# Performance work log

Hardware: AMD Instinct MI355X
Metric: run time of the kernel (lower is better)

The kernel has to match this reference:

```python
import jax, jax.numpy as jnp
import numpy as np

C = 8            # feat_channel
B, K, H, W = 8, 32, 128, 128
CW = (C + 2) * C + C + C * C + C + C + 1  # 169


def setup_inputs() -> dict:
    key = jax.random.key(0)
    k1, k2, k3, k4, k5 = jax.random.split(key, 5)
    seg_feat = jax.random.normal(k1, (B, C, H, W), jnp.float32)
    conv_weight = jax.random.normal(k2, (B, CW, H, W), jnp.float32) * 0.1
    mask = jax.random.randint(k3, (B, K), 0, 2).astype(jnp.int32)
    ind = jax.random.randint(k4, (B, K), 0, H * W).astype(jnp.int64)
    target = jax.random.uniform(k5, (B, K, H, W), jnp.float32)
    return {"seg_feat": seg_feat, "conv_weight": conv_weight, "mask": mask,
            "ind": ind, "target": target}


def reference(seg_feat, conv_weight, mask, ind, target):
    b, c, h, w = seg_feat.shape
    k = ind.shape[1]
    # gather_feature(conv_weight, ind, use_transform=True): [B,CW,H,W] -> [B,HW,CW] -> gather -> [B,K,CW]
    cw = conv_weight.reshape(b, -1, h * w).transpose(0, 2, 1)
    weight = jnp.take_along_axis(cw, ind[:, :, None], axis=1)  # [B,K,CW]

    sizes = [(c + 2) * c, c, c * c, c, c, 1]
    splits = np.cumsum(sizes)[:-1]
    c1w, c1b, c2w, c2b, c3w, c3b = jnp.split(weight, splits, axis=-1)
    c1w = c1w.reshape(b, k, c, c + 2)   # per-object 1x1 conv weights
    c2w = c2w.reshape(b, k, c, c)
    c3w = c3w.reshape(b, k, 1, c)

    x = (ind % w).astype(jnp.float32)
    y = (ind // w).astype(jnp.float32)
    y_grid, x_grid = jnp.meshgrid(jnp.arange(h, dtype=jnp.float32),
                                  jnp.arange(w, dtype=jnp.float32), indexing='ij')
    x_rel = (x_grid[None, None] - x[:, :, None, None]) / w   # [B,K,H,W]
    y_rel = (y_grid[None, None] - y[:, :, None, None]) / h

    feat = jnp.concatenate([
        jnp.broadcast_to(seg_feat[:, None], (b, k, c, h, w)),
        x_rel[:, :, None], y_rel[:, :, None]], axis=2)       # [B,K,C+2,H,W]

    feat = jax.nn.relu(jnp.einsum('bkoc,bkchw->bkohw', c1w, feat) + c1b[..., None, None])
    feat = jax.nn.relu(jnp.einsum('bkoc,bkchw->bkohw', c2w, feat) + c2b[..., None, None])
    pred = jax.nn.sigmoid(jnp.einsum('bkoc,bkchw->bkohw', c3w, feat)
                          + c3b[..., None, None])[:, :, 0]    # [B,K,H,W]

    m = mask.astype(jnp.float32)[:, :, None, None]
    p = pred * m
    t = target * m
    smooth = 1.0
    inter = jnp.sum(p * t, axis=(1, 2, 3))
    denom = jnp.sum(p * p, axis=(1, 2, 3)) + jnp.sum(t * t, axis=(1, 2, 3)) + smooth
    per_img = 1.0 - (2.0 * inter + smooth) / denom
    return jnp.mean(per_img)   # sum over images / valid_batch_size (all valid)
```

## Files before the change

### kernel.cpp

```cpp
#include <hip/hip_runtime.h>

#define C8     8
#define KOBJ   32
#define BIMG   8
#define WW     128
#define HH     128
#define HWPIX  16384
#define CWN    169
#define PIX    8
#define GRIDX  8
#define NBLK_PER_B (KOBJ * GRIDX)
#define NXCD   8


__global__ __launch_bounds__(256) void mask_head_kernel(
    const float* __restrict__ seg_feat,
    const float* __restrict__ conv_weight,
    const int* __restrict__ mask,
    const long long* __restrict__ ind,
    const float* __restrict__ target,
    float* __restrict__ partial)
{
    const int id   = blockIdx.x;
    const int b    = id & (NXCD - 1);
    const int rest = id >> 3;
    const int k    = rest & (KOBJ - 1);
    const int tile = rest >> 5;

    const int t    = threadIdx.x;
    const int blockFlat = (b * KOBJ + k) * GRIDX + tile;
    float* my = partial + blockFlat * 3;

    if (mask[b * KOBJ + k] == 0) {
        if (t == 0) { my[0] = 0.f; my[1] = 0.f; my[2] = 0.f; }
        return;
    }

    __shared__ __align__(16) float l1w[C8][12];
    __shared__ __align__(16) float l2w[C8][C8];
    __shared__ __align__(16) float l1b[C8];
    __shared__ __align__(16) float l2b[C8];
    __shared__ __align__(16) float l3w[C8];
    __shared__ float l3b_s;
    __shared__ float red[4][3];

    const int idx = (int)ind[b * KOBJ + k];
    if (t < CWN) {
        const float v = conv_weight[(b * CWN + t) * HWPIX + idx];
        if (t < 80)       { l1w[t / 10][t % 10] = v; }
        else if (t < 88)  { l1b[t - 80] = v; }
        else if (t < 152) { const int u = t - 88; l2w[u >> 3][u & 7] = v; }
        else if (t < 160) { l2b[t - 152] = v; }
        else if (t < 168) { l3w[t - 160] = v; }
        else              { l3b_s = v; }
    }
    __syncthreads();

    const float cx = (float)(idx & (WW - 1));
    const float cy = (float)(idx >> 7);

    const float* seg = seg_feat + b * C8 * HWPIX;
    const float* tgt = target + (b * KOBJ + k) * HWPIX;

    const int p0 = (tile * 256 + t) * PIX;

    const float4 t4a = *reinterpret_cast<const float4*>(&tgt[p0]);
    const float4 t4b = *reinterpret_cast<const float4*>(&tgt[p0 + 4]);

    const float sy  = ((float)(p0 >> 7) - cy) * (1.0f / 128.0f);
    const float sx0 = ((float)(p0 & (WW - 1)) - cx) * (1.0f / 128.0f);
    float sx[PIX];
#pragma unroll
    for (int i = 0; i < PIX; ++i) sx[i] = sx0 + (float)i * (1.0f / 128.0f);

    float f[C8][PIX];
#pragma unroll
    for (int c = 0; c < C8; ++c) {
        const float4 a = *reinterpret_cast<const float4*>(&seg[c * HWPIX + p0]);
        const float4 d = *reinterpret_cast<const float4*>(&seg[c * HWPIX + p0 + 4]);
        f[c][0] = a.x; f[c][1] = a.y; f[c][2] = a.z; f[c][3] = a.w;
        f[c][4] = d.x; f[c][5] = d.y; f[c][6] = d.z; f[c][7] = d.w;
    }

    float h1[C8][PIX];
#pragma unroll
    for (int o = 0; o < C8; ++o) {
        const float4 wa = *reinterpret_cast<const float4*>(&l1w[o][0]);
        const float4 wb = *reinterpret_cast<const float4*>(&l1w[o][4]);
        const float4 wc = *reinterpret_cast<const float4*>(&l1w[o][8]);
        const float base = fmaf(wc.y, sy, l1b[o]);
#pragma unroll
        for (int i = 0; i < PIX; ++i) {
            float a = fmaf(wc.x, sx[i], base);
            a = fmaf(wa.x, f[0][i], a);
            a = fmaf(wa.y, f[1][i], a);
            a = fmaf(wa.z, f[2][i], a);
            a = fmaf(wa.w, f[3][i], a);
            a = fmaf(wb.x, f[4][i], a);
            a = fmaf(wb.y, f[5][i], a);
            a = fmaf(wb.z, f[6][i], a);
            a = fmaf(wb.w, f[7][i], a);
            h1[o][i] = fmaxf(a, 0.f);
        }
    }

    float h2[C8][PIX];
#pragma unroll
    for (int o = 0; o < C8; ++o) {
        const float4 wa = *reinterpret_cast<const float4*>(&l2w[o][0]);
        const float4 wb = *reinterpret_cast<const float4*>(&l2w[o][4]);
        const float bias = l2b[o];
#pragma unroll
        for (int i = 0; i < PIX; ++i) {
            float a = bias;
            a = fmaf(wa.x, h1[0][i], a);
            a = fmaf(wa.y, h1[1][i], a);
            a = fmaf(wa.z, h1[2][i], a);
            a = fmaf(wa.w, h1[3][i], a);
            a = fmaf(wb.x, h1[4][i], a);
            a = fmaf(wb.y, h1[5][i], a);
            a = fmaf(wb.z, h1[6][i], a);
            a = fmaf(wb.w, h1[7][i], a);
            h2[o][i] = fmaxf(a, 0.f);
        }
    }

    const float4 wa = *reinterpret_cast<const float4*>(&l3w[0]);
    const float4 wb = *reinterpret_cast<const float4*>(&l3w[4]);
    const float b3 = l3b_s;
    float tv[PIX];
    tv[0] = t4a.x; tv[1] = t4a.y; tv[2] = t4a.z; tv[3] = t4a.w;
    tv[4] = t4b.x; tv[5] = t4b.y; tv[6] = t4b.z; tv[7] = t4b.w;

    float s_pt = 0.f, s_pp = 0.f, s_tt = 0.f;
#pragma unroll
    for (int i = 0; i < PIX; ++i) {
        float z = b3;
        z = fmaf(wa.x, h2[0][i], z);
        z = fmaf(wa.y, h2[1][i], z);
        z = fmaf(wa.z, h2[2][i], z);
        z = fmaf(wa.w, h2[3][i], z);
        z = fmaf(wb.x, h2[4][i], z);
        z = fmaf(wb.y, h2[5][i], z);
        z = fmaf(wb.z, h2[6][i], z);
        z = fmaf(wb.w, h2[7][i], z);
        const float e    = __expf(-z);
        const float pred = __builtin_amdgcn_rcpf(1.0f + e);
        s_pt = fmaf(pred, tv[i], s_pt);
        s_pp = fmaf(pred, pred, s_pp);
        s_tt = fmaf(tv[i], tv[i], s_tt);
    }

#pragma unroll
    for (int off = 32; off > 0; off >>= 1) {
        s_pt += __shfl_down(s_pt, off);
        s_pp += __shfl_down(s_pp, off);
        s_tt += __shfl_down(s_tt, off);
    }
    const int wid = t >> 6;
    if ((t & 63) == 0) { red[wid][0] = s_pt; red[wid][1] = s_pp; red[wid][2] = s_tt; }
    __syncthreads();
    if (t == 0) {
        float a = 0.f, b2 = 0.f, c2 = 0.f;
#pragma unroll
        for (int i = 0; i < 4; ++i) { a += red[i][0]; b2 += red[i][1]; c2 += red[i][2]; }
        my[0] = a; my[1] = b2; my[2] = c2;
    }
}

__global__ __launch_bounds__(512) void finalize_kernel(
    const float* __restrict__ partial, float* __restrict__ out)
{
    const int t    = threadIdx.x;
    const int b    = t >> 6;
    const int lane = t & 63;

    float pt = 0.f, pp = 0.f, tt = 0.f;
    for (int e = lane; e < NBLK_PER_B; e += 64) {
        const float* q = partial + (b * NBLK_PER_B + e) * 3;
        pt += q[0]; pp += q[1]; tt += q[2];
    }
#pragma unroll
    for (int off = 32; off > 0; off >>= 1) {
        pt += __shfl_down(pt, off);
        pp += __shfl_down(pp, off);
        tt += __shfl_down(tt, off);
    }
    __shared__ float per[BIMG];
    if (lane == 0) {
        per[b] = 1.0f - (2.0f * pt + 1.0f) / (pp + tt + 1.0f);
    }
    __syncthreads();
    if (t == 0) {
        float s = 0.f;
#pragma unroll
        for (int i = 0; i < BIMG; ++i) s += per[i];
        out[0] = s * (1.0f / (float)BIMG);
    }
}

extern "C" void kernel_launch(void* const* d_in, const int* in_sizes, int n_in,
                              void* d_out, int out_size, void* d_ws, size_t ws_size,
                              hipStream_t stream) {
    const float*     seg  = (const float*)d_in[0];
    const float*     cw   = (const float*)d_in[1];
    const int*       mask = (const int*)d_in[2];
    const long long* ind  = (const long long*)d_in[3];
    const float*     tgt  = (const float*)d_in[4];
    float* out     = (float*)d_out;
    float* partial = (float*)d_ws;

    mask_head_kernel<<<dim3(BIMG * KOBJ * GRIDX), 256, 0, stream>>>(seg, cw, mask, ind, tgt, partial);
    finalize_kernel<<<1, 512, 0, stream>>>(partial, out);
}
```

Baseline: 22.38 us.

## Use 2D row-tiled blocks processing four pixel batches per thread with fewer blocks

Halves the grid to 1024 blocks, each covering 32 rows of one object with 256 threads looping four times over 4-pixel strips, instead of 2048 blocks of 8 contiguous pixels per thread. The block index now puts k in the low bits so that blocks of the same image run near each other, which should help seg_feat stay in cache. The per-block weight gather and setup are amortized over more pixels, and register use per iteration drops, with a launch bound hint of 3 blocks per CU. The finalize kernel is shrunk to 256 threads with a loop over images. The trade-off is less parallelism per block and more serialized work per thread.

```diff
diff --git a/kernel.cpp b/kernel.cpp
--- a/kernel.cpp
+++ b/kernel.cpp
@@ -4,16 +4,14 @@
 #define KOBJ   32
 #define BIMG   8
 #define WW     128
-#define HH     128
 #define HWPIX  16384
 #define CWN    169
-#define PIX    8
-#define GRIDX  8
-#define NBLK_PER_B (KOBJ * GRIDX)
-#define NXCD   8
-
-
-__global__ __launch_bounds__(256) void mask_head_kernel(
+#define TQ     4
+#define SLOTS_PER_B (KOBJ * TQ)
+#define NB     (BIMG * SLOTS_PER_B)
+
+
+__global__ __launch_bounds__(256, 3) void mask_head_kernel(
     const float* __restrict__ seg_feat,
     const float* __restrict__ conv_weight,
     const int* __restrict__ mask,
@@ -22,23 +20,22 @@
     float* __restrict__ partial)
 {
     const int id   = blockIdx.x;
-    const int b    = id & (NXCD - 1);
-    const int rest = id >> 3;
-    const int k    = rest & (KOBJ - 1);
-    const int tile = rest >> 5;
-
+    const int k    = id & (KOBJ - 1);
+    const int rest = id >> 5;
+    const int b    = rest & (BIMG - 1);
+    const int t4   = rest >> 3;
     const int t    = threadIdx.x;
-    const int blockFlat = (b * KOBJ + k) * GRIDX + tile;
-    float* my = partial + blockFlat * 3;
+
+    float* my = partial + (b * SLOTS_PER_B + k * TQ + t4) * 3;
 
     if (mask[b * KOBJ + k] == 0) {
-        if (t == 0) { my[0] = 0.f; my[1] = 0.f; my[2] = 0.f; }
+        if (t < 3) my[t] = 0.f;
         return;
     }
 
     __shared__ __align__(16) float l1w[C8][12];
+    __shared__ __align__(16) float l1b[C8];
     __shared__ __align__(16) float l2w[C8][C8];
-    __shared__ __align__(16) float l1b[C8];
     __shared__ __align__(16) float l2b[C8];
     __shared__ __align__(16) float l3w[C8];
     __shared__ float l3b_s;
@@ -62,93 +59,95 @@
     const float* seg = seg_feat + b * C8 * HWPIX;
     const float* tgt = target + (b * KOBJ + k) * HWPIX;
 
-    const int p0 = (tile * 256 + t) * PIX;
-
-    const float4 t4a = *reinterpret_cast<const float4*>(&tgt[p0]);
-    const float4 t4b = *reinterpret_cast<const float4*>(&tgt[p0 + 4]);
-
-    const float sy  = ((float)(p0 >> 7) - cy) * (1.0f / 128.0f);
-    const float sx0 = ((float)(p0 & (WW - 1)) - cx) * (1.0f / 128.0f);
-    float sx[PIX];
-#pragma unroll
-    for (int i = 0; i < PIX; ++i) sx[i] = sx0 + (float)i * (1.0f / 128.0f);
-
-    float f[C8][PIX];
-#pragma unroll
-    for (int c = 0; c < C8; ++c) {
-        const float4 a = *reinterpret_cast<const float4*>(&seg[c * HWPIX + p0]);
-        const float4 d = *reinterpret_cast<const float4*>(&seg[c * HWPIX + p0 + 4]);
-        f[c][0] = a.x; f[c][1] = a.y; f[c][2] = a.z; f[c][3] = a.w;
-        f[c][4] = d.x; f[c][5] = d.y; f[c][6] = d.z; f[c][7] = d.w;
-    }
-
-    float h1[C8][PIX];
-#pragma unroll
-    for (int o = 0; o < C8; ++o) {
-        const float4 wa = *reinterpret_cast<const float4*>(&l1w[o][0]);
-        const float4 wb = *reinterpret_cast<const float4*>(&l1w[o][4]);
-        const float4 wc = *reinterpret_cast<const float4*>(&l1w[o][8]);
-        const float base = fmaf(wc.y, sy, l1b[o]);
-#pragma unroll
-        for (int i = 0; i < PIX; ++i) {
-            float a = fmaf(wc.x, sx[i], base);
-            a = fmaf(wa.x, f[0][i], a);
-            a = fmaf(wa.y, f[1][i], a);
-            a = fmaf(wa.z, f[2][i], a);
-            a = fmaf(wa.w, f[3][i], a);
-            a = fmaf(wb.x, f[4][i], a);
-            a = fmaf(wb.y, f[5][i], a);
-            a = fmaf(wb.z, f[6][i], a);
-            a = fmaf(wb.w, f[7][i], a);
-            h1[o][i] = fmaxf(a, 0.f);
-        }
-    }
-
-    float h2[C8][PIX];
-#pragma unroll
-    for (int o = 0; o < C8; ++o) {
-        const float4 wa = *reinterpret_cast<const float4*>(&l2w[o][0]);
-        const float4 wb = *reinterpret_cast<const float4*>(&l2w[o][4]);
-        const float bias = l2b[o];
-#pragma unroll
-        for (int i = 0; i < PIX; ++i) {
-            float a = bias;
-            a = fmaf(wa.x, h1[0][i], a);
-            a = fmaf(wa.y, h1[1][i], a);
-            a = fmaf(wa.z, h1[2][i], a);
-            a = fmaf(wa.w, h1[3][i], a);
-            a = fmaf(wb.x, h1[4][i], a);
-            a = fmaf(wb.y, h1[5][i], a);
-            a = fmaf(wb.z, h1[6][i], a);
-            a = fmaf(wb.w, h1[7][i], a);
-            h2[o][i] = fmaxf(a, 0.f);
-        }
-    }
-
-    const float4 wa = *reinterpret_cast<const float4*>(&l3w[0]);
-    const float4 wb = *reinterpret_cast<const float4*>(&l3w[4]);
-    const float b3 = l3b_s;
-    float tv[PIX];
-    tv[0] = t4a.x; tv[1] = t4a.y; tv[2] = t4a.z; tv[3] = t4a.w;
-    tv[4] = t4b.x; tv[5] = t4b.y; tv[6] = t4b.z; tv[7] = t4b.w;
+    const int colbase = (t & 31) * 4;
+    const int rsub    = t >> 5;
+
+    float sx[4];
+#pragma unroll
+    for (int i = 0; i < 4; ++i) sx[i] = ((float)(colbase + i) - cx) * (1.0f / 128.0f);
 
     float s_pt = 0.f, s_pp = 0.f, s_tt = 0.f;
-#pragma unroll
-    for (int i = 0; i < PIX; ++i) {
-        float z = b3;
-        z = fmaf(wa.x, h2[0][i], z);
-        z = fmaf(wa.y, h2[1][i], z);
-        z = fmaf(wa.z, h2[2][i], z);
-        z = fmaf(wa.w, h2[3][i], z);
-        z = fmaf(wb.x, h2[4][i], z);
-        z = fmaf(wb.y, h2[5][i], z);
-        z = fmaf(wb.z, h2[6][i], z);
-        z = fmaf(wb.w, h2[7][i], z);
-        const float e    = __expf(-z);
-        const float pred = __builtin_amdgcn_rcpf(1.0f + e);
-        s_pt = fmaf(pred, tv[i], s_pt);
-        s_pp = fmaf(pred, pred, s_pp);
-        s_tt = fmaf(tv[i], tv[i], s_tt);
+
+#pragma unroll
+    for (int b4 = 0; b4 < 4; ++b4) {
+        const int row = t4 * 32 + b4 * 8 + rsub;
+        const int px  = row * WW + colbase;
+
+        const float4 tv4 = *reinterpret_cast<const float4*>(&tgt[px]);
+        const float sy = ((float)row - cy) * (1.0f / 128.0f);
+
+        float f[C8][4];
+#pragma unroll
+        for (int c = 0; c < C8; ++c) {
+            const float4 a = *reinterpret_cast<const float4*>(&seg[c * HWPIX + px]);
+            f[c][0] = a.x; f[c][1] = a.y; f[c][2] = a.z; f[c][3] = a.w;
+        }
+
+        float h1[C8][4];
+#pragma unroll
+        for (int o = 0; o < C8; ++o) {
+            const float4 wa = *reinterpret_cast<const float4*>(&l1w[o][0]);
+            const float4 wb = *reinterpret_cast<const float4*>(&l1w[o][4]);
+            const float4 wc = *reinterpret_cast<const float4*>(&l1w[o][8]);
+            const float base = fmaf(wc.y, sy, l1b[o]);
+#pragma unroll
+            for (int i = 0; i < 4; ++i) {
+                float a = fmaf(wc.x, sx[i], base);
+                a = fmaf(wa.x, f[0][i], a);
+                a = fmaf(wa.y, f[1][i], a);
+                a = fmaf(wa.z, f[2][i], a);
+                a = fmaf(wa.w, f[3][i], a);
+                a = fmaf(wb.x, f[4][i], a);
+                a = fmaf(wb.y, f[5][i], a);
+                a = fmaf(wb.z, f[6][i], a);
+                a = fmaf(wb.w, f[7][i], a);
+                h1[o][i] = fmaxf(a, 0.f);
+            }
+        }
+
+        float h2[C8][4];
+#pragma unroll
+        for (int o = 0; o < C8; ++o) {
+            const float4 wa = *reinterpret_cast<const float4*>(&l2w[o][0]);
+            const float4 wb = *reinterpret_cast<const float4*>(&l2w[o][4]);
+            const float bias = l2b[o];
+#pragma unroll
+            for (int i = 0; i < 4; ++i) {
+                float a = bias;
+                a = fmaf(wa.x, h1[0][i], a);
+                a = fmaf(wa.y, h1[1][i], a);
+                a = fmaf(wa.z, h1[2][i], a);
+                a = fmaf(wa.w, h1[3][i], a);
+                a = fmaf(wb.x, h1[4][i], a);
+                a = fmaf(wb.y, h1[5][i], a);
+                a = fmaf(wb.z, h1[6][i], a);
+                a = fmaf(wb.w, h1[7][i], a);
+                h2[o][i] = fmaxf(a, 0.f);
+            }
+        }
+
+        const float4 wa = *reinterpret_cast<const float4*>(&l3w[0]);
+        const float4 wb = *reinterpret_cast<const float4*>(&l3w[4]);
+        const float b3 = l3b_s;
+        float tvv[4];
+        tvv[0] = tv4.x; tvv[1] = tv4.y; tvv[2] = tv4.z; tvv[3] = tv4.w;
+#pragma unroll
+        for (int i = 0; i < 4; ++i) {
+            float z = b3;
+            z = fmaf(wa.x, h2[0][i], z);
+            z = fmaf(wa.y, h2[1][i], z);
+            z = fmaf(wa.z, h2[2][i], z);
+            z = fmaf(wa.w, h2[3][i], z);
+            z = fmaf(wb.x, h2[4][i], z);
+            z = fmaf(wb.y, h2[5][i], z);
+            z = fmaf(wb.z, h2[6][i], z);
+            z = fmaf(wb.w, h2[7][i], z);
+            const float e    = __expf(-z);
+            const float pred = __builtin_amdgcn_rcpf(1.0f + e);
+            s_pt = fmaf(pred, tvv[i], s_pt);
+            s_pp = fmaf(pred, pred, s_pp);
+            s_tt = fmaf(tvv[i], tvv[i], s_tt);
+        }
     }
 
 #pragma unroll
@@ -168,27 +167,29 @@
     }
 }
 
-__global__ __launch_bounds__(512) void finalize_kernel(
+__global__ __launch_bounds__(256) void finalize_kernel(
     const float* __restrict__ partial, float* __restrict__ out)
 {
     const int t    = threadIdx.x;
-    const int b    = t >> 6;
+    const int w    = t >> 6;
     const int lane = t & 63;
-
-    float pt = 0.f, pp = 0.f, tt = 0.f;
-    for (int e = lane; e < NBLK_PER_B; e += 64) {
-        const float* q = partial + (b * NBLK_PER_B + e) * 3;
-        pt += q[0]; pp += q[1]; tt += q[2];
-    }
-#pragma unroll
-    for (int off = 32; off > 0; off >>= 1) {
-        pt += __shfl_down(pt, off);
-        pp += __shfl_down(pp, off);
-        tt += __shfl_down(tt, off);
-    }
     __shared__ float per[BIMG];
-    if (lane == 0) {
-        per[b] = 1.0f - (2.0f * pt + 1.0f) / (pp + tt + 1.0f);
+
+    for (int img = w; img < BIMG; img += 4) {
+        const float* base = partial + img * SLOTS_PER_B * 3;
+        float pt = 0.f, pp = 0.f, tt = 0.f;
+        for (int s = lane; s < SLOTS_PER_B; s += 64) {
+            pt += base[s * 3 + 0];
+            pp += base[s * 3 + 1];
+            tt += base[s * 3 + 2];
+        }
+#pragma unroll
+        for (int off = 32; off > 0; off >>= 1) {
+            pt += __shfl_down(pt, off);
+            pp += __shfl_down(pp, off);
+            tt += __shfl_down(tt, off);
+        }
+        if (lane == 0) per[img] = 1.0f - (2.0f * pt + 1.0f) / (pp + tt + 1.0f);
     }
     __syncthreads();
     if (t == 0) {
@@ -210,6 +211,6 @@
     float* out     = (float*)d_out;
     float* partial = (float*)d_ws;
 
-    mask_head_kernel<<<dim3(BIMG * KOBJ * GRIDX), 256, 0, stream>>>(seg, cw, mask, ind, tgt, partial);
-    finalize_kernel<<<1, 512, 0, stream>>>(partial, out);
+    mask_head_kernel<<<dim3(NB), 256, 0, stream>>>(seg, cw, mask, ind, tgt, partial);
+    finalize_kernel<<<1, 256, 0, stream>>>(partial, out);
 }
```

New measurement: 75.47 us. 237% more time.
